# Performance work log

Measured on AMD Instinct MI355X. Metric: run time of the kernel, lower is better.

The kernel has to match this reference:

```python
import jax, jax.numpy as jnp
import numpy as np
import math

B, C, HH, WW = 4, 256, 64, 64
NUM_HEADS = 4
GROUPS = 8
EPS = 1e-5


def setup_inputs() -> dict:
    key = jax.random.key(0)
    k1, k2, k3 = jax.random.split(key, 3)
    x = jax.random.normal(k1, (B, C, HH, WW), dtype=jnp.float32)
    gn_w = jnp.ones((C,), dtype=jnp.float32)
    gn_b = jnp.zeros((C,), dtype=jnp.float32)
    qkv_w = jax.random.normal(k2, (3 * C, C), dtype=jnp.float32) * (1.0 / math.sqrt(C))
    qkv_b = jnp.zeros((3 * C,), dtype=jnp.float32)
    proj_w = jax.random.normal(k3, (C, C), dtype=jnp.float32) * (1.0 / math.sqrt(C))
    proj_b = jnp.zeros((C,), dtype=jnp.float32)
    return {"x": x, "gn_w": gn_w, "gn_b": gn_b, "qkv_w": qkv_w,
            "qkv_b": qkv_b, "proj_w": proj_w, "proj_b": proj_b}


def reference(x, gn_w, gn_b, qkv_w, qkv_b, proj_w, proj_b):
    b, c, h, w = x.shape
    nh = NUM_HEADS
    d = c // nh          # head dim = 64
    s = h * w            # sequence length = 4096

    # GroupNorm(8, c): normalize over (c//G, h, w) per group, biased variance
    xg = x.reshape(b, GROUPS, c // GROUPS, h, w)
    mu = xg.mean(axis=(2, 3, 4), keepdims=True)
    var = xg.var(axis=(2, 3, 4), keepdims=True)
    xn = ((xg - mu) * jax.lax.rsqrt(var + EPS)).reshape(b, c, h, w)
    xn = xn * gn_w[None, :, None, None] + gn_b[None, :, None, None]

    # 1x1 conv QKV == channel-wise matmul
    qkv = jnp.einsum('oc,bchw->bohw', qkv_w, xn) + qkv_b[None, :, None, None]
    qkv = qkv.reshape(b, 3, nh, d, s)
    q = jnp.transpose(qkv[:, 0], (0, 1, 3, 2))  # [b, nh, s, d]
    k = jnp.transpose(qkv[:, 1], (0, 1, 3, 2))
    v = jnp.transpose(qkv[:, 2], (0, 1, 3, 2))

    scale = 1.0 / math.sqrt(d)
    attn = jnp.einsum('bhqd,bhkd->bhqk', q, k) * scale  # [b, nh, s, s]
    attn = jax.nn.softmax(attn, axis=-1)
    out = jnp.einsum('bhqk,bhkd->bhqd', attn, v)        # [b, nh, s, d]

    out = jnp.transpose(out, (0, 1, 3, 2)).reshape(b, c, h, w)
    out = jnp.einsum('oc,bchw->bohw', proj_w, out) + proj_b[None, :, None, None]
    return out + x
```

## Files before the change

kernel.cpp:

```cpp
#include <hip/hip_runtime.h>
#include <hip/hip_bf16.h>

#define B_ 4
#define C_ 256
#define S_ 4096
#define NH_ 4
#define HD_ 64
#define LOG2E 1.4426950408889634f
#define QSC 0.18033688011112042f

typedef __attribute__((ext_vector_type(8))) short short8;
typedef __attribute__((ext_vector_type(4))) short short4v;
typedef __attribute__((ext_vector_type(4))) float f32x4;
typedef __attribute__((ext_vector_type(16))) float f32x16;
typedef __attribute__((ext_vector_type(4))) unsigned uint4v;

static __device__ __forceinline__ short f2bf(float f) {
  unsigned u = __builtin_bit_cast(unsigned, f);
  u += 0x7fffu + ((u >> 16) & 1u);
  return (short)(u >> 16);
}
static __device__ __forceinline__ float bf2f(short h) {
  unsigned u = ((unsigned)(unsigned short)h) << 16;
  return __builtin_bit_cast(float, u);
}

#if __has_builtin(__builtin_amdgcn_exp2f)
#define EXP2(x) __builtin_amdgcn_exp2f(x)
#else
#define EXP2(x) exp2f(x)
#endif

static __device__ __forceinline__ unsigned pkbf(float a, float b) {
  unsigned r;
  asm("v_cvt_pk_bf16_f32 %0, %1, %2" : "=v"(r) : "v"(a), "v"(b));
  return r;
}
static __device__ __forceinline__ void pl32swap(unsigned& a, unsigned& b) {
  asm volatile("v_permlane32_swap_b32 %0, %1" : "+v"(a), "+v"(b));
}
static __device__ __forceinline__ void gl_lds16(const short* g, char* l) {
  __builtin_amdgcn_global_load_lds(
      (const __attribute__((address_space(1))) void*)g,
      (__attribute__((address_space(3))) void*)l, 16, 0, 0);
}

__global__ __launch_bounds__(256) void k_pre(const float* __restrict__ x,
                                             const float* __restrict__ wq,
                                             const float* __restrict__ wp,
                                             float* __restrict__ part,
                                             short* __restrict__ oq,
                                             short* __restrict__ op) {
  int t = threadIdx.x;
  const float* p = x + (size_t)blockIdx.x * 16384;
  float s = 0.f, ss = 0.f;
  const float4* p4 = reinterpret_cast<const float4*>(p);
  for (int i = t; i < 4096; i += 256) {
    float4 v = p4[i];
    s += v.x + v.y + v.z + v.w;
    ss += v.x * v.x + v.y * v.y + v.z * v.z + v.w * v.w;
  }
  for (int m = 1; m < 64; m <<= 1) {
    s += __shfl_xor(s, m, 64);
    ss += __shfl_xor(ss, m, 64);
  }
  __shared__ float rs[4], rss[4];
  int w = t >> 6;
  if ((t & 63) == 0) { rs[w] = s; rss[w] = ss; }
  {
    int i = (blockIdx.x * 256 + t) * 4;
    const int n1 = 768 * 256;
    float sc = 1.f;
    const float* src;
    short* dst;
    if (i < n1) {
      src = wq + i; dst = oq + i;
      if (i < 256 * 256) sc = QSC;
    } else {
      src = wp + (i - n1); dst = op + (i - n1);
    }
    float4 v = *reinterpret_cast<const float4*>(src);
    short4v o;
    o[0] = f2bf(v.x * sc); o[1] = f2bf(v.y * sc);
    o[2] = f2bf(v.z * sc); o[3] = f2bf(v.w * sc);
    *reinterpret_cast<short4v*>(dst) = o;
  }
  __syncthreads();
  if (t == 0) {
    part[2 * blockIdx.x] = rs[0] + rs[1] + rs[2] + rs[3];
    part[2 * blockIdx.x + 1] = rss[0] + rss[1] + rss[2] + rss[3];
  }
}

__global__ __launch_bounds__(256) void k_gn_apply(const float* __restrict__ x,
                                                  const float* __restrict__ gw,
                                                  const float* __restrict__ gb,
                                                  const float* __restrict__ part,
                                                  short* __restrict__ xnt) {
  int st = blockIdx.x;
  int ct = blockIdx.y;
  int b = blockIdx.z;
  int t = threadIdx.x;
  __shared__ short T[64 * 72];
  __shared__ float smu[2], sri[2];
  int c0 = ct * 64, s0 = st * 64;
  if (t < 2) {
    int g = (c0 >> 5) + t;
    int base = b * 64 + g * 8;
    float s = 0.f, ss = 0.f;
    for (int j = 0; j < 8; j++) {
      s += part[2 * (base + j)];
      ss += part[2 * (base + j) + 1];
    }
    float inv = 1.f / (32.f * S_);
    float mu = s * inv;
    float var = ss * inv - mu * mu;
    smu[t] = mu;
    sri[t] = rsqrtf(var + 1e-5f);
  }
  __syncthreads();
  int r4 = t >> 4;
  int f4 = t & 15;
  for (int p = 0; p < 4; p++) {
    int r = p * 16 + r4;
    int c = c0 + r;
    int gl = r >> 5;
    float mu = smu[gl];
    float ri = sri[gl];
    float A = gw[c] * ri;
    float Bb = gb[c] - mu * A;
    float4 v = *reinterpret_cast<const float4*>(x + ((size_t)(b * C_ + c)) * S_ + s0 + f4 * 4);
    int sb = f4 * 4;
    T[(sb + 0) * 72 + r] = f2bf(v.x * A + Bb);
    T[(sb + 1) * 72 + r] = f2bf(v.y * A + Bb);
    T[(sb + 2) * 72 + r] = f2bf(v.z * A + Bb);
    T[(sb + 3) * 72 + r] = f2bf(v.w * A + Bb);
  }
  __syncthreads();
  for (int it = 0; it < 2; it++) {
    int cch = t + it * 256;
    int sl = cch >> 3, c8 = cch & 7;
    short8 v = *reinterpret_cast<short8*>(&T[sl * 72 + c8 * 8]);
    *reinterpret_cast<short8*>(xnt + ((size_t)(b * S_ + s0 + sl)) * C_ + c0 + c8 * 8) = v;
  }
}

template <int MODE, int NSP>
__global__ __launch_bounds__(256) void k_gemm(const short* __restrict__ Wbf,
                                              const short* __restrict__ Xt,
                                              const float* __restrict__ bias,
                                              const float* __restrict__ xres,
                                              short* __restrict__ q_sd,
                                              short* __restrict__ k_sd,
                                              short* __restrict__ v_ds,
                                              long op_stride,
                                              const float* __restrict__ lbufg,
                                              float* __restrict__ outp) {
  int tn = blockIdx.x;
  int tm = blockIdx.y;
  int b = blockIdx.z;
  int t = threadIdx.x;
  __shared__ short lds[4 * 64 * 72];
  short* Al = lds;
  short* Bl = lds + 128 * 40;
  int w = t >> 6, lane = t & 63;
  int wr = w >> 1, wc = w & 1;
  int l15 = lane & 15, l4 = lane >> 4;

  f32x4 acc[4][4];
  for (int m = 0; m < 4; m++)
    for (int n = 0; n < 4; n++)
      for (int j = 0; j < 4; j++) acc[m][n][j] = 0.f;

  const short* Arow = Wbf + (size_t)(tm * 128) * 256;
  const short* Brow = Xt + ((size_t)b * S_ + tn * 128) * 256;

  for (int kk = 0; kk < 256; kk += 32) {
    __syncthreads();
    for (int i = 0; i < 2; i++) {
      int cch = t + i * 256;
      int r = cch >> 2, c4 = cch & 3;
      short8 va = *reinterpret_cast<const short8*>(Arow + (size_t)r * 256 + kk + c4 * 8);
      *reinterpret_cast<short8*>(&Al[r * 40 + c4 * 8]) = va;
      short8 vbv;
      if (MODE == 0) {
        vbv = *reinterpret_cast<const short8*>(Brow + (size_t)r * 256 + kk + c4 * 8);
      } else {
        int c = kk + c4 * 8;
        int bh2 = b * 4 + (c >> 6);
        int d = c & 63;
        int s_glob = tn * 128 + r;
        size_t ro = ((size_t)bh2 * S_ + s_glob) * HD_ + d;
        float a8[8] = {0.f, 0.f, 0.f, 0.f, 0.f, 0.f, 0.f, 0.f};
        float l = 0.f;
#pragma unroll
        for (int i2 = 0; i2 < NSP; i2++) {
          short8 pv = *reinterpret_cast<const short8*>(Xt + (size_t)i2 * op_stride + ro);
#pragma unroll
          for (int j = 0; j < 8; j++) a8[j] += bf2f(pv[j]);
          l += lbufg[(size_t)(i2 * 16 + bh2) * S_ + s_glob];
        }
        float inv = 1.f / l;
#pragma unroll
        for (int j = 0; j < 8; j++) vbv[j] = f2bf(a8[j] * inv);
      }
      *reinterpret_cast<short8*>(&Bl[r * 40 + c4 * 8]) = vbv;
    }
    __syncthreads();
    short8 af[4], bf[4];
    for (int mt = 0; mt < 4; mt++)
      af[mt] = *reinterpret_cast<short8*>(&Al[(wr * 64 + mt * 16 + l15) * 40 + l4 * 8]);
    for (int nt = 0; nt < 4; nt++)
      bf[nt] = *reinterpret_cast<short8*>(&Bl[(wc * 64 + nt * 16 + l15) * 40 + l4 * 8]);
    for (int mt = 0; mt < 4; mt++)
      for (int nt = 0; nt < 4; nt++)
        acc[mt][nt] = __builtin_amdgcn_mfma_f32_16x16x32_bf16(af[mt], bf[nt], acc[mt][nt], 0, 0, 0);
  }
  __syncthreads();

  if (MODE == 0) {
    int o_base = tm * 128 + wr * 64;
    int tt = o_base >> 8;
    int h = (o_base >> 6) & 3;
    int s_base = tn * 128 + wc * 64;
    int bh = b * NH_ + h;
    if (tt == 2) {
      for (int mt = 0; mt < 4; mt++)
        for (int nt = 0; nt < 4; nt++)
          for (int i = 0; i < 4; i++) {
            int o = o_base + mt * 16 + l4 * 4 + i;
            int dd = o & 63;
            int s = s_base + nt * 16 + l15;
            float val = acc[mt][nt][i] + bias[o];
            v_ds[((size_t)bh * HD_ + dd) * S_ + s] = f2bf(val);
          }
    } else {
      float bsc = (tt == 0) ? QSC : 1.f;
      short* T = lds + w * (64 * 72);
      for (int mt = 0; mt < 4; mt++)
        for (int nt = 0; nt < 4; nt++)
          for (int i = 0; i < 4; i++) {
            int o = o_base + mt * 16 + l4 * 4 + i;
            int dd = mt * 16 + l4 * 4 + i;
            int sl = nt * 16 + l15;
            float val = acc[mt][nt][i] + bias[o] * bsc;
            T[sl * 72 + dd] = f2bf(val);
          }
      short* dst = (tt == 0) ? q_sd : k_sd;
      for (int it = 0; it < 8; it++) {
        int cch = lane + it * 64;
        int sl = cch >> 3, c8 = cch & 7;
        short8 v = *reinterpret_cast<short8*>(&T[sl * 72 + c8 * 8]);
        *reinterpret_cast<short8*>(dst + ((size_t)bh * S_ + s_base + sl) * HD_ + c8 * 8) = v;
      }
    }
  } else {
    for (int mt = 0; mt < 4; mt++) {
      int o = tm * 128 + wr * 64 + mt * 16 + l4 * 4;
      for (int nt = 0; nt < 4; nt++) {
        int s = tn * 128 + wc * 64 + nt * 16 + l15;
        for (int i = 0; i < 4; i++) {
          size_t off = ((size_t)(b * C_ + o + i)) * S_ + s;
          outp[off] = acc[mt][nt][i] + bias[o + i] + xres[off];
        }
      }
    }
  }
}

__global__ __launch_bounds__(256, 2) void k_attn(const short* __restrict__ q_sd,
                                                 const short* __restrict__ k_sd,
                                                 const short* __restrict__ v_ds,
                                                 short* __restrict__ op_base,
                                                 long op_stride,
                                                 float* __restrict__ lbuf,
                                                 int ntile, int lg) {
  int bid = blockIdx.x;
  int sk = bid & ((1 << lg) - 1);
  int bh = (bid >> lg) & 15;
  int qt = bid >> (lg + 4);
  int t = threadIdx.x, w = t >> 6, lane = t & 63;
  int l31 = lane & 31, hi = lane >> 5, hi8 = hi * 8;
  int qb = qt * 256 + w * 64;

  __shared__ char smem[32768];

  int wb = __builtin_amdgcn_readfirstlane(w) << 10;

  int r8 = t >> 3, s8 = t & 7;
  int sw8 = (s8 ^ (r8 & 7)) * 8;
  const short* kb = k_sd + ((size_t)bh * S_ + (size_t)sk * ntile * 64) * HD_;
  const short* vbg = v_ds + (size_t)bh * HD_ * S_ + sk * ntile * 64;
  int koff0 = r8 * 64 + sw8;
  int koff1 = koff0 + 32 * 64;
  size_t voff0 = (size_t)r8 * S_ + sw8;
  size_t voff1 = voff0 + (size_t)32 * S_;

#define STAGE(bsel, ti)                                                        \
  do {                                                                         \
    const short* kt_ = kb + (size_t)(ti) * (64 * HD_);                         \
    const short* vt_ = vbg + (ti) * 64;                                        \
    char* lb_ = smem + ((bsel) << 14) + wb;                                    \
    gl_lds16(kt_ + koff0, lb_);                                                \
    gl_lds16(kt_ + koff1, lb_ + 4096);                                         \
    gl_lds16(vt_ + voff0, lb_ + 8192);                                         \
    gl_lds16(vt_ + voff1, lb_ + 12288);                                        \
  } while (0)

  const short* qpA = q_sd + ((size_t)bh * S_ + qb + l31) * HD_ + hi8;
  short8 qfA[4], qfB[4];
#pragma unroll
  for (int sl = 0; sl < 4; sl++) {
    qfA[sl] = *reinterpret_cast<const short8*>(qpA + sl * 16);
    qfB[sl] = *reinterpret_cast<const short8*>(qpA + 32 * HD_ + sl * 16);
  }

  int x7 = l31 & 7;
  int rb0 = l31 * 128;

  f32x16 OA0, OA1, OB0, OB1;
#pragma unroll
  for (int r = 0; r < 16; r++) { OA0[r] = 0.f; OA1[r] = 0.f; OB0[r] = 0.f; OB1[r] = 0.f; }
  float lA = 0.f, lB = 0.f;

  STAGE(0, 0);
  if (ntile > 1) STAGE(1, 1);
  asm volatile("s_waitcnt vmcnt(0)" ::: "memory");
  __builtin_amdgcn_s_barrier();
  asm volatile("" ::: "memory");

#define MKPA(pa, s0, s1)                                                       \
  do {                                                                         \
    unsigned c0 = pkbf(s0[0], s0[1]), c1 = pkbf(s0[2], s0[3]);                 \
    unsigned c2 = pkbf(s0[4], s0[5]), c3 = pkbf(s0[6], s0[7]);                 \
    pl32swap(c0, c2); pl32swap(c1, c3);                                        \
    uint4v u0; u0[0] = c0; u0[1] = c1; u0[2] = c2; u0[3] = c3;                 \
    pa[0] = __builtin_bit_cast(short8, u0);                                    \
    unsigned c4 = pkbf(s0[8], s0[9]), c5 = pkbf(s0[10], s0[11]);               \
    unsigned c6 = pkbf(s0[12], s0[13]), c7 = pkbf(s0[14], s0[15]);             \
    pl32swap(c4, c6); pl32swap(c5, c7);                                        \
    uint4v u1; u1[0] = c4; u1[1] = c5; u1[2] = c6; u1[3] = c7;                 \
    pa[1] = __builtin_bit_cast(short8, u1);                                    \
    unsigned d0 = pkbf(s1[0], s1[1]), d1 = pkbf(s1[2], s1[3]);                 \
    unsigned d2 = pkbf(s1[4], s1[5]), d3 = pkbf(s1[6], s1[7]);                 \
    pl32swap(d0, d2); pl32swap(d1, d3);                                        \
    uint4v u2; u2[0] = d0; u2[1] = d1; u2[2] = d2; u2[3] = d3;                 \
    pa[2] = __builtin_bit_cast(short8, u2);                                    \
    unsigned d4 = pkbf(s1[8], s1[9]), d5 = pkbf(s1[10], s1[11]);               \
    unsigned d6 = pkbf(s1[12], s1[13]), d7 = pkbf(s1[14], s1[15]);             \
    pl32swap(d4, d6); pl32swap(d5, d7);                                        \
    uint4v u3; u3[0] = d4; u3[1] = d5; u3[2] = d6; u3[3] = d7;                 \
    pa[3] = __builtin_bit_cast(short8, u3);                                    \
  } while (0)

  for (int it = 0; it < ntile; it++) {
    char* cur = smem + ((it & 1) << 14);

    f32x16 sA0, sA1, sB0, sB1;
#pragma unroll
    for (int r = 0; r < 16; r++) { sA0[r] = 0.f; sA1[r] = 0.f; sB0[r] = 0.f; sB1[r] = 0.f; }
    __builtin_amdgcn_s_setprio(1);
#pragma unroll
    for (int sl = 0; sl < 4; sl++) {
      int so = ((sl * 2 + hi) ^ x7) << 4;
      short8 kf0 = *reinterpret_cast<short8*>(cur + rb0 + so);
      short8 kf1 = *reinterpret_cast<short8*>(cur + 4096 + rb0 + so);
      sA0 = __builtin_amdgcn_mfma_f32_32x32x16_bf16(kf0, qfA[sl], sA0, 0, 0, 0);
      sB0 = __builtin_amdgcn_mfma_f32_32x32x16_bf16(kf0, qfB[sl], sB0, 0, 0, 0);
      sA1 = __builtin_amdgcn_mfma_f32_32x32x16_bf16(kf1, qfA[sl], sA1, 0, 0, 0);
      sB1 = __builtin_amdgcn_mfma_f32_32x32x16_bf16(kf1, qfB[sl], sB1, 0, 0, 0);
    }
    __builtin_amdgcn_s_setprio(0);

#pragma unroll
    for (int r = 0; r < 16; r++) sA0[r] = EXP2(sA0[r]);
#pragma unroll
    for (int r = 0; r < 16; r++) sA1[r] = EXP2(sA1[r]);
#pragma unroll
    for (int r = 0; r < 16; r++) sB0[r] = EXP2(sB0[r]);
#pragma unroll
    for (int r = 0; r < 16; r++) sB1[r] = EXP2(sB1[r]);
    {
      float a0 = 0.f, a1 = 0.f, a2 = 0.f, a3 = 0.f;
      float b0 = 0.f, b1 = 0.f, b2 = 0.f, b3 = 0.f;
#pragma unroll
      for (int r = 0; r < 16; r += 4) {
        a0 += sA0[r]; a1 += sA0[r + 1]; a2 += sA0[r + 2]; a3 += sA0[r + 3];
        a0 += sA1[r]; a1 += sA1[r + 1]; a2 += sA1[r + 2]; a3 += sA1[r + 3];
        b0 += sB0[r]; b1 += sB0[r + 1]; b2 += sB0[r + 2]; b3 += sB0[r + 3];
        b0 += sB1[r]; b1 += sB1[r + 1]; b2 += sB1[r + 2]; b3 += sB1[r + 3];
      }
      float rsA = (a0 + a1) + (a2 + a3);
      float rsB = (b0 + b1) + (b2 + b3);
      rsA += __shfl_xor(rsA, 32, 64);
      rsB += __shfl_xor(rsB, 32, 64);
      lA += rsA;
      lB += rsB;
    }

    short8 paA[4], paB[4];
    MKPA(paA, sA0, sA1);
    MKPA(paB, sB0, sB1);

    __builtin_amdgcn_s_setprio(1);
#pragma unroll
    for (int ks = 0; ks < 4; ks++) {
      int so = ((ks * 2 + hi) ^ x7) << 4;
      short8 vf0 = *reinterpret_cast<short8*>(cur + 8192 + rb0 + so);
      short8 vf1 = *reinterpret_cast<short8*>(cur + 12288 + rb0 + so);
      OA0 = __builtin_amdgcn_mfma_f32_32x32x16_bf16(vf0, paA[ks], OA0, 0, 0, 0);
      OB0 = __builtin_amdgcn_mfma_f32_32x32x16_bf16(vf0, paB[ks], OB0, 0, 0, 0);
      OA1 = __builtin_amdgcn_mfma_f32_32x32x16_bf16(vf1, paA[ks], OA1, 0, 0, 0);
      OB1 = __builtin_amdgcn_mfma_f32_32x32x16_bf16(vf1, paB[ks], OB1, 0, 0, 0);
    }
    __builtin_amdgcn_s_setprio(0);

    if (it + 1 < ntile) {
      __builtin_amdgcn_s_barrier();
      if (it + 2 < ntile) {
        STAGE(it & 1, it + 2);
        asm volatile("s_waitcnt vmcnt(4)" ::: "memory");
      } else {
        asm volatile("s_waitcnt vmcnt(0)" ::: "memory");
      }
      __builtin_amdgcn_s_barrier();
      asm volatile("" ::: "memory");
    }
  }

  short* optrA = op_base + (size_t)sk * op_stride + ((size_t)bh * S_ + qb + l31) * HD_;
  short* optrB = optrA + 32 * HD_;
#pragma unroll
  for (int qd = 0; qd < 4; qd++) {
    short4v a0, a1, b0v, b1v;
#pragma unroll
    for (int i = 0; i < 4; i++) {
      a0[i] = f2bf(OA0[qd * 4 + i]);
      a1[i] = f2bf(OA1[qd * 4 + i]);
      b0v[i] = f2bf(OB0[qd * 4 + i]);
      b1v[i] = f2bf(OB1[qd * 4 + i]);
    }
    int d0 = qd * 8 + hi * 4;
    *reinterpret_cast<short4v*>(optrA + d0) = a0;
    *reinterpret_cast<short4v*>(optrA + 32 + d0) = a1;
    *reinterpret_cast<short4v*>(optrB + d0) = b0v;
    *reinterpret_cast<short4v*>(optrB + 32 + d0) = b1v;
  }
  if (hi == 0) {
    lbuf[(size_t)(sk * 16 + bh) * S_ + qb + l31] = lA;
    lbuf[(size_t)(sk * 16 + bh) * S_ + qb + 32 + l31] = lB;
  }
#undef STAGE
#undef MKPA
}

extern "C" void kernel_launch(void* const* d_in, const int* in_sizes, int n_in,
                              void* d_out, int out_size, void* d_ws, size_t ws_size,
                              hipStream_t stream) {
  const float* x      = (const float*)d_in[0];
  const float* gn_w   = (const float*)d_in[1];
  const float* gn_b   = (const float*)d_in[2];
  const float* qkv_w  = (const float*)d_in[3];
  const float* qkv_b  = (const float*)d_in[4];
  const float* proj_w = (const float*)d_in[5];
  const float* proj_b = (const float*)d_in[6];
  char* ws = (char*)d_ws;
  float* part  = (float*)(ws + 2048);
  short* wqkv  = (short*)(ws + 4096);
  short* wproj = (short*)(ws + 397312);
  short* xnt   = (short*)(ws + 528384);
  short* q_sd  = (short*)(ws + 8916992);
  short* k_sd  = (short*)(ws + 17305600);
  short* v_ds  = (short*)(ws + 25694208);
  float* outp  = (float*)d_out;

  const size_t need4 = 42471424ULL + 4ULL * 8388608ULL + 4ULL * 16 * 4096 * 4;
  int lg;
  short* op_base;
  long op_stride;
  float* lbuf;
  if (ws_size >= need4) {
    lg = 2;
    op_base = (short*)(ws + 42471424);
    op_stride = 8388608 / 2;
    lbuf = (float*)(ws + 42471424 + 4ULL * 8388608ULL);
  } else {
    lg = 1;
    op_base = xnt;
    op_stride = (42471424 - 528384) / 2;
    lbuf = (float*)(ws + 50860032);
  }
  int NS = 1 << lg;

  k_pre<<<256, 256, 0, stream>>>(x, qkv_w, proj_w, part, wqkv, wproj);
  k_gn_apply<<<dim3(64, 4, 4), 256, 0, stream>>>(x, gn_w, gn_b, part, xnt);
  k_gemm<0, 0><<<dim3(32, 6, 4), 256, 0, stream>>>(wqkv, xnt, qkv_b, nullptr, q_sd, k_sd, v_ds,
                                                   0, nullptr, nullptr);
  k_attn<<<16 * 16 * NS, 256, 0, stream>>>(q_sd, k_sd, v_ds, op_base, op_stride, lbuf,
                                           64 >> lg, lg);
  if (NS == 4)
    k_gemm<1, 4><<<dim3(32, 2, 4), 256, 0, stream>>>(wproj, op_base, proj_b, x, nullptr, nullptr,
                                                     nullptr, op_stride, lbuf, outp);
  else
    k_gemm<1, 2><<<dim3(32, 2, 4), 256, 0, stream>>>(wproj, op_base, proj_b, x, nullptr, nullptr,
                                                     nullptr, op_stride, lbuf, outp);
}
```

Baseline: 135.1 us.

## Halve attention query tile per wave and double grid for higher occupancy

Each wave now processes 32 query rows instead of 64, cutting accumulator and score registers in half, and launch bounds are raised to four blocks per CU. The grid doubles to cover the same queries. The aim is more resident waves to hide latency, at the cost of loading each K/V tile twice as often, halving the reuse of staged K/V per block.

```diff
diff --git a/kernel.cpp b/kernel.cpp
--- a/kernel.cpp
+++ b/kernel.cpp
@@ -268,7 +268,7 @@
   }
 }
 
-__global__ __launch_bounds__(256, 2) void k_attn(const short* __restrict__ q_sd,
+__global__ __launch_bounds__(256, 4) void k_attn(const short* __restrict__ q_sd,
                                                  const short* __restrict__ k_sd,
                                                  const short* __restrict__ v_ds,
                                                  short* __restrict__ op_base,
@@ -281,7 +281,7 @@
   int qt = bid >> (lg + 4);
   int t = threadIdx.x, w = t >> 6, lane = t & 63;
   int l31 = lane & 31, hi = lane >> 5, hi8 = hi * 8;
-  int qb = qt * 256 + w * 64;
+  int qb = qt * 128 + w * 32;
 
   __shared__ char smem[32768];
 
@@ -307,21 +307,18 @@
     gl_lds16(vt_ + voff1, lb_ + 12288);                                        \
   } while (0)
 
-  const short* qpA = q_sd + ((size_t)bh * S_ + qb + l31) * HD_ + hi8;
-  short8 qfA[4], qfB[4];
-#pragma unroll
-  for (int sl = 0; sl < 4; sl++) {
-    qfA[sl] = *reinterpret_cast<const short8*>(qpA + sl * 16);
-    qfB[sl] = *reinterpret_cast<const short8*>(qpA + 32 * HD_ + sl * 16);
-  }
+  const short* qp = q_sd + ((size_t)bh * S_ + qb + l31) * HD_ + hi8;
+  short8 qf[4];
+#pragma unroll
+  for (int sl = 0; sl < 4; sl++) qf[sl] = *reinterpret_cast<const short8*>(qp + sl * 16);
 
   int x7 = l31 & 7;
   int rb0 = l31 * 128;
 
-  f32x16 OA0, OA1, OB0, OB1;
-#pragma unroll
-  for (int r = 0; r < 16; r++) { OA0[r] = 0.f; OA1[r] = 0.f; OB0[r] = 0.f; OB1[r] = 0.f; }
-  float lA = 0.f, lB = 0.f;
+  f32x16 Oacc0, Oacc1;
+#pragma unroll
+  for (int r = 0; r < 16; r++) { Oacc0[r] = 0.f; Oacc1[r] = 0.f; }
+  float l_run = 0.f;
 
   STAGE(0, 0);
   if (ntile > 1) STAGE(1, 1);
@@ -329,78 +326,62 @@
   __builtin_amdgcn_s_barrier();
   asm volatile("" ::: "memory");
 
-#define MKPA(pa, s0, s1)                                                       \
-  do {                                                                         \
-    unsigned c0 = pkbf(s0[0], s0[1]), c1 = pkbf(s0[2], s0[3]);                 \
-    unsigned c2 = pkbf(s0[4], s0[5]), c3 = pkbf(s0[6], s0[7]);                 \
-    pl32swap(c0, c2); pl32swap(c1, c3);                                        \
-    uint4v u0; u0[0] = c0; u0[1] = c1; u0[2] = c2; u0[3] = c3;                 \
-    pa[0] = __builtin_bit_cast(short8, u0);                                    \
-    unsigned c4 = pkbf(s0[8], s0[9]), c5 = pkbf(s0[10], s0[11]);               \
-    unsigned c6 = pkbf(s0[12], s0[13]), c7 = pkbf(s0[14], s0[15]);             \
-    pl32swap(c4, c6); pl32swap(c5, c7);                                        \
-    uint4v u1; u1[0] = c4; u1[1] = c5; u1[2] = c6; u1[3] = c7;                 \
-    pa[1] = __builtin_bit_cast(short8, u1);                                    \
-    unsigned d0 = pkbf(s1[0], s1[1]), d1 = pkbf(s1[2], s1[3]);                 \
-    unsigned d2 = pkbf(s1[4], s1[5]), d3 = pkbf(s1[6], s1[7]);                 \
-    pl32swap(d0, d2); pl32swap(d1, d3);                                        \
-    uint4v u2; u2[0] = d0; u2[1] = d1; u2[2] = d2; u2[3] = d3;                 \
-    pa[2] = __builtin_bit_cast(short8, u2);                                    \
-    unsigned d4 = pkbf(s1[8], s1[9]), d5 = pkbf(s1[10], s1[11]);               \
-    unsigned d6 = pkbf(s1[12], s1[13]), d7 = pkbf(s1[14], s1[15]);             \
-    pl32swap(d4, d6); pl32swap(d5, d7);                                        \
-    uint4v u3; u3[0] = d4; u3[1] = d5; u3[2] = d6; u3[3] = d7;                 \
-    pa[3] = __builtin_bit_cast(short8, u3);                                    \
-  } while (0)
-
   for (int it = 0; it < ntile; it++) {
     char* cur = smem + ((it & 1) << 14);
 
-    f32x16 sA0, sA1, sB0, sB1;
-#pragma unroll
-    for (int r = 0; r < 16; r++) { sA0[r] = 0.f; sA1[r] = 0.f; sB0[r] = 0.f; sB1[r] = 0.f; }
+    f32x16 st0, st1;
+#pragma unroll
+    for (int r = 0; r < 16; r++) { st0[r] = 0.f; st1[r] = 0.f; }
     __builtin_amdgcn_s_setprio(1);
 #pragma unroll
     for (int sl = 0; sl < 4; sl++) {
       int so = ((sl * 2 + hi) ^ x7) << 4;
       short8 kf0 = *reinterpret_cast<short8*>(cur + rb0 + so);
       short8 kf1 = *reinterpret_cast<short8*>(cur + 4096 + rb0 + so);
-      sA0 = __builtin_amdgcn_mfma_f32_32x32x16_bf16(kf0, qfA[sl], sA0, 0, 0, 0);
-      sB0 = __builtin_amdgcn_mfma_f32_32x32x16_bf16(kf0, qfB[sl], sB0, 0, 0, 0);
-      sA1 = __builtin_amdgcn_mfma_f32_32x32x16_bf16(kf1, qfA[sl], sA1, 0, 0, 0);
-      sB1 = __builtin_amdgcn_mfma_f32_32x32x16_bf16(kf1, qfB[sl], sB1, 0, 0, 0);
+      st0 = __builtin_amdgcn_mfma_f32_32x32x16_bf16(kf0, qf[sl], st0, 0, 0, 0);
+      st1 = __builtin_amdgcn_mfma_f32_32x32x16_bf16(kf1, qf[sl], st1, 0, 0, 0);
     }
     __builtin_amdgcn_s_setprio(0);
 
 #pragma unroll
-    for (int r = 0; r < 16; r++) sA0[r] = EXP2(sA0[r]);
-#pragma unroll
-    for (int r = 0; r < 16; r++) sA1[r] = EXP2(sA1[r]);
-#pragma unroll
-    for (int r = 0; r < 16; r++) sB0[r] = EXP2(sB0[r]);
-#pragma unroll
-    for (int r = 0; r < 16; r++) sB1[r] = EXP2(sB1[r]);
+    for (int r = 0; r < 16; r++) st0[r] = EXP2(st0[r]);
+#pragma unroll
+    for (int r = 0; r < 16; r++) st1[r] = EXP2(st1[r]);
     {
       float a0 = 0.f, a1 = 0.f, a2 = 0.f, a3 = 0.f;
-      float b0 = 0.f, b1 = 0.f, b2 = 0.f, b3 = 0.f;
 #pragma unroll
       for (int r = 0; r < 16; r += 4) {
-        a0 += sA0[r]; a1 += sA0[r + 1]; a2 += sA0[r + 2]; a3 += sA0[r + 3];
-        a0 += sA1[r]; a1 += sA1[r + 1]; a2 += sA1[r + 2]; a3 += sA1[r + 3];
-        b0 += sB0[r]; b1 += sB0[r + 1]; b2 += sB0[r + 2]; b3 += sB0[r + 3];
-        b0 += sB1[r]; b1 += sB1[r + 1]; b2 += sB1[r + 2]; b3 += sB1[r + 3];
+        a0 += st0[r]; a1 += st0[r + 1]; a2 += st0[r + 2]; a3 += st0[r + 3];
+        a0 += st1[r]; a1 += st1[r + 1]; a2 += st1[r + 2]; a3 += st1[r + 3];
       }
-      float rsA = (a0 + a1) + (a2 + a3);
-      float rsB = (b0 + b1) + (b2 + b3);
-      rsA += __shfl_xor(rsA, 32, 64);
-      rsB += __shfl_xor(rsB, 32, 64);
-      lA += rsA;
-      lB += rsB;
-    }
-
-    short8 paA[4], paB[4];
-    MKPA(paA, sA0, sA1);
-    MKPA(paB, sB0, sB1);
+      float rs = (a0 + a1) + (a2 + a3);
+      rs += __shfl_xor(rs, 32, 64);
+      l_run += rs;
+    }
+
+    short8 pa[4];
+    {
+      unsigned c0 = pkbf(st0[0], st0[1]), c1 = pkbf(st0[2], st0[3]);
+      unsigned c2 = pkbf(st0[4], st0[5]), c3 = pkbf(st0[6], st0[7]);
+      pl32swap(c0, c2); pl32swap(c1, c3);
+      uint4v u0; u0[0] = c0; u0[1] = c1; u0[2] = c2; u0[3] = c3;
+      pa[0] = __builtin_bit_cast(short8, u0);
+      unsigned c4 = pkbf(st0[8], st0[9]), c5 = pkbf(st0[10], st0[11]);
+      unsigned c6 = pkbf(st0[12], st0[13]), c7 = pkbf(st0[14], st0[15]);
+      pl32swap(c4, c6); pl32swap(c5, c7);
+      uint4v u1; u1[0] = c4; u1[1] = c5; u1[2] = c6; u1[3] = c7;
+      pa[1] = __builtin_bit_cast(short8, u1);
+      unsigned d0 = pkbf(st1[0], st1[1]), d1 = pkbf(st1[2], st1[3]);
+      unsigned d2 = pkbf(st1[4], st1[5]), d3 = pkbf(st1[6], st1[7]);
+      pl32swap(d0, d2); pl32swap(d1, d3);
+      uint4v u2; u2[0] = d0; u2[1] = d1; u2[2] = d2; u2[3] = d3;
+      pa[2] = __builtin_bit_cast(short8, u2);
+      unsigned d4 = pkbf(st1[8], st1[9]), d5 = pkbf(st1[10], st1[11]);
+      unsigned d6 = pkbf(st1[12], st1[13]), d7 = pkbf(st1[14], st1[15]);
+      pl32swap(d4, d6); pl32swap(d5, d7);
+      uint4v u3; u3[0] = d4; u3[1] = d5; u3[2] = d6; u3[3] = d7;
+      pa[3] = __builtin_bit_cast(short8, u3);
+    }
 
     __builtin_amdgcn_s_setprio(1);
 #pragma unroll
@@ -408,10 +389,8 @@
       int so = ((ks * 2 + hi) ^ x7) << 4;
       short8 vf0 = *reinterpret_cast<short8*>(cur + 8192 + rb0 + so);
       short8 vf1 = *reinterpret_cast<short8*>(cur + 12288 + rb0 + so);
-      OA0 = __builtin_amdgcn_mfma_f32_32x32x16_bf16(vf0, paA[ks], OA0, 0, 0, 0);
-      OB0 = __builtin_amdgcn_mfma_f32_32x32x16_bf16(vf0, paB[ks], OB0, 0, 0, 0);
-      OA1 = __builtin_amdgcn_mfma_f32_32x32x16_bf16(vf1, paA[ks], OA1, 0, 0, 0);
-      OB1 = __builtin_amdgcn_mfma_f32_32x32x16_bf16(vf1, paB[ks], OB1, 0, 0, 0);
+      Oacc0 = __builtin_amdgcn_mfma_f32_32x32x16_bf16(vf0, pa[ks], Oacc0, 0, 0, 0);
+      Oacc1 = __builtin_amdgcn_mfma_f32_32x32x16_bf16(vf1, pa[ks], Oacc1, 0, 0, 0);
     }
     __builtin_amdgcn_s_setprio(0);
 
@@ -428,30 +407,21 @@
     }
   }
 
-  short* optrA = op_base + (size_t)sk * op_stride + ((size_t)bh * S_ + qb + l31) * HD_;
-  short* optrB = optrA + 32 * HD_;
+  short* optr = op_base + (size_t)sk * op_stride + ((size_t)bh * S_ + qb + l31) * HD_;
 #pragma unroll
   for (int qd = 0; qd < 4; qd++) {
-    short4v a0, a1, b0v, b1v;
+    short4v o0, o1;
 #pragma unroll
     for (int i = 0; i < 4; i++) {
-      a0[i] = f2bf(OA0[qd * 4 + i]);
-      a1[i] = f2bf(OA1[qd * 4 + i]);
-      b0v[i] = f2bf(OB0[qd * 4 + i]);
-      b1v[i] = f2bf(OB1[qd * 4 + i]);
+      o0[i] = f2bf(Oacc0[qd * 4 + i]);
+      o1[i] = f2bf(Oacc1[qd * 4 + i]);
     }
     int d0 = qd * 8 + hi * 4;
-    *reinterpret_cast<short4v*>(optrA + d0) = a0;
-    *reinterpret_cast<short4v*>(optrA + 32 + d0) = a1;
-    *reinterpret_cast<short4v*>(optrB + d0) = b0v;
-    *reinterpret_cast<short4v*>(optrB + 32 + d0) = b1v;
-  }
-  if (hi == 0) {
-    lbuf[(size_t)(sk * 16 + bh) * S_ + qb + l31] = lA;
-    lbuf[(size_t)(sk * 16 + bh) * S_ + qb + 32 + l31] = lB;
-  }
+    *reinterpret_cast<short4v*>(optr + d0) = o0;
+    *reinterpret_cast<short4v*>(optr + 32 + d0) = o1;
+  }
+  if (hi == 0) lbuf[(size_t)(sk * 16 + bh) * S_ + qb + l31] = l_run;
 #undef STAGE
-#undef MKPA
 }
 
 extern "C" void kernel_launch(void* const* d_in, const int* in_sizes, int n_in,
@@ -496,7 +466,7 @@
   k_gn_apply<<<dim3(64, 4, 4), 256, 0, stream>>>(x, gn_w, gn_b, part, xnt);
   k_gemm<0, 0><<<dim3(32, 6, 4), 256, 0, stream>>>(wqkv, xnt, qkv_b, nullptr, q_sd, k_sd, v_ds,
                                                    0, nullptr, nullptr);
-  k_attn<<<16 * 16 * NS, 256, 0, stream>>>(q_sd, k_sd, v_ds, op_base, op_stride, lbuf,
+  k_attn<<<32 * 16 * NS, 256, 0, stream>>>(q_sd, k_sd, v_ds, op_base, op_stride, lbuf,
                                            64 >> lg, lg);
   if (NS == 4)
     k_gemm<1, 4><<<dim3(32, 2, 4), 256, 0, stream>>>(wproj, op_base, proj_b, x, nullptr, nullptr,
```

Measured after the change: 139.5 us. 1.03x slower.

## Split attention KV tile into two halves to cut registers and raise occupancy

Applied to the files above, without the earlier changes.

Each 64-key tile is now processed as two 32-key halves, each running QK^T, exp2, row-sum, bf16 packing and PV MFMA, so only two score accumulators are live instead of four. Launch bounds go from 2 to 3 waves per SIMD to use the lower register pressure, the cross-half row-sum shuffle is moved out of the loop to once at the end, and V offsets become 32-bit ints. The risk is spills under the tighter register budget and less MFMA/exp overlap within a wave.

```diff
diff --git a/kernel.cpp b/kernel.cpp
--- a/kernel.cpp
+++ b/kernel.cpp
@@ -268,7 +268,7 @@
   }
 }
 
-__global__ __launch_bounds__(256, 2) void k_attn(const short* __restrict__ q_sd,
+__global__ __launch_bounds__(256, 3) void k_attn(const short* __restrict__ q_sd,
                                                  const short* __restrict__ k_sd,
                                                  const short* __restrict__ v_ds,
                                                  short* __restrict__ op_base,
@@ -293,8 +293,8 @@
   const short* vbg = v_ds + (size_t)bh * HD_ * S_ + sk * ntile * 64;
   int koff0 = r8 * 64 + sw8;
   int koff1 = koff0 + 32 * 64;
-  size_t voff0 = (size_t)r8 * S_ + sw8;
-  size_t voff1 = voff0 + (size_t)32 * S_;
+  int voff0 = r8 * S_ + sw8;
+  int voff1 = voff0 + 32 * S_;
 
 #define STAGE(bsel, ti)                                                        \
   do {                                                                         \
@@ -329,91 +329,80 @@
   __builtin_amdgcn_s_barrier();
   asm volatile("" ::: "memory");
 
-#define MKPA(pa, s0, s1)                                                       \
-  do {                                                                         \
-    unsigned c0 = pkbf(s0[0], s0[1]), c1 = pkbf(s0[2], s0[3]);                 \
-    unsigned c2 = pkbf(s0[4], s0[5]), c3 = pkbf(s0[6], s0[7]);                 \
-    pl32swap(c0, c2); pl32swap(c1, c3);                                        \
-    uint4v u0; u0[0] = c0; u0[1] = c1; u0[2] = c2; u0[3] = c3;                 \
-    pa[0] = __builtin_bit_cast(short8, u0);                                    \
-    unsigned c4 = pkbf(s0[8], s0[9]), c5 = pkbf(s0[10], s0[11]);               \
-    unsigned c6 = pkbf(s0[12], s0[13]), c7 = pkbf(s0[14], s0[15]);             \
-    pl32swap(c4, c6); pl32swap(c5, c7);                                        \
-    uint4v u1; u1[0] = c4; u1[1] = c5; u1[2] = c6; u1[3] = c7;                 \
-    pa[1] = __builtin_bit_cast(short8, u1);                                    \
-    unsigned d0 = pkbf(s1[0], s1[1]), d1 = pkbf(s1[2], s1[3]);                 \
-    unsigned d2 = pkbf(s1[4], s1[5]), d3 = pkbf(s1[6], s1[7]);                 \
-    pl32swap(d0, d2); pl32swap(d1, d3);                                        \
-    uint4v u2; u2[0] = d0; u2[1] = d1; u2[2] = d2; u2[3] = d3;                 \
-    pa[2] = __builtin_bit_cast(short8, u2);                                    \
-    unsigned d4 = pkbf(s1[8], s1[9]), d5 = pkbf(s1[10], s1[11]);               \
-    unsigned d6 = pkbf(s1[12], s1[13]), d7 = pkbf(s1[14], s1[15]);             \
-    pl32swap(d4, d6); pl32swap(d5, d7);                                        \
-    uint4v u3; u3[0] = d4; u3[1] = d5; u3[2] = d6; u3[3] = d7;                 \
-    pa[3] = __builtin_bit_cast(short8, u3);                                    \
-  } while (0)
-
   for (int it = 0; it < ntile; it++) {
     char* cur = smem + ((it & 1) << 14);
 
-    f32x16 sA0, sA1, sB0, sB1;
-#pragma unroll
-    for (int r = 0; r < 16; r++) { sA0[r] = 0.f; sA1[r] = 0.f; sB0[r] = 0.f; sB1[r] = 0.f; }
-    __builtin_amdgcn_s_setprio(1);
-#pragma unroll
-    for (int sl = 0; sl < 4; sl++) {
-      int so = ((sl * 2 + hi) ^ x7) << 4;
-      short8 kf0 = *reinterpret_cast<short8*>(cur + rb0 + so);
-      short8 kf1 = *reinterpret_cast<short8*>(cur + 4096 + rb0 + so);
-      sA0 = __builtin_amdgcn_mfma_f32_32x32x16_bf16(kf0, qfA[sl], sA0, 0, 0, 0);
-      sB0 = __builtin_amdgcn_mfma_f32_32x32x16_bf16(kf0, qfB[sl], sB0, 0, 0, 0);
-      sA1 = __builtin_amdgcn_mfma_f32_32x32x16_bf16(kf1, qfA[sl], sA1, 0, 0, 0);
-      sB1 = __builtin_amdgcn_mfma_f32_32x32x16_bf16(kf1, qfB[sl], sB1, 0, 0, 0);
-    }
-    __builtin_amdgcn_s_setprio(0);
-
-#pragma unroll
-    for (int r = 0; r < 16; r++) sA0[r] = EXP2(sA0[r]);
-#pragma unroll
-    for (int r = 0; r < 16; r++) sA1[r] = EXP2(sA1[r]);
-#pragma unroll
-    for (int r = 0; r < 16; r++) sB0[r] = EXP2(sB0[r]);
-#pragma unroll
-    for (int r = 0; r < 16; r++) sB1[r] = EXP2(sB1[r]);
-    {
-      float a0 = 0.f, a1 = 0.f, a2 = 0.f, a3 = 0.f;
-      float b0 = 0.f, b1 = 0.f, b2 = 0.f, b3 = 0.f;
-#pragma unroll
-      for (int r = 0; r < 16; r += 4) {
-        a0 += sA0[r]; a1 += sA0[r + 1]; a2 += sA0[r + 2]; a3 += sA0[r + 3];
-        a0 += sA1[r]; a1 += sA1[r + 1]; a2 += sA1[r + 2]; a3 += sA1[r + 3];
-        b0 += sB0[r]; b1 += sB0[r + 1]; b2 += sB0[r + 2]; b3 += sB0[r + 3];
-        b0 += sB1[r]; b1 += sB1[r + 1]; b2 += sB1[r + 2]; b3 += sB1[r + 3];
-      }
-      float rsA = (a0 + a1) + (a2 + a3);
-      float rsB = (b0 + b1) + (b2 + b3);
-      rsA += __shfl_xor(rsA, 32, 64);
-      rsB += __shfl_xor(rsB, 32, 64);
-      lA += rsA;
-      lB += rsB;
-    }
-
-    short8 paA[4], paB[4];
-    MKPA(paA, sA0, sA1);
-    MKPA(paB, sB0, sB1);
-
-    __builtin_amdgcn_s_setprio(1);
-#pragma unroll
-    for (int ks = 0; ks < 4; ks++) {
-      int so = ((ks * 2 + hi) ^ x7) << 4;
-      short8 vf0 = *reinterpret_cast<short8*>(cur + 8192 + rb0 + so);
-      short8 vf1 = *reinterpret_cast<short8*>(cur + 12288 + rb0 + so);
-      OA0 = __builtin_amdgcn_mfma_f32_32x32x16_bf16(vf0, paA[ks], OA0, 0, 0, 0);
-      OB0 = __builtin_amdgcn_mfma_f32_32x32x16_bf16(vf0, paB[ks], OB0, 0, 0, 0);
-      OA1 = __builtin_amdgcn_mfma_f32_32x32x16_bf16(vf1, paA[ks], OA1, 0, 0, 0);
-      OB1 = __builtin_amdgcn_mfma_f32_32x32x16_bf16(vf1, paB[ks], OB1, 0, 0, 0);
-    }
-    __builtin_amdgcn_s_setprio(0);
+#pragma unroll
+    for (int h = 0; h < 2; h++) {
+      f32x16 SA, SB;
+#pragma unroll
+      for (int r = 0; r < 16; r++) { SA[r] = 0.f; SB[r] = 0.f; }
+      __builtin_amdgcn_s_setprio(1);
+#pragma unroll
+      for (int sl = 0; sl < 4; sl++) {
+        int so = ((sl * 2 + hi) ^ x7) << 4;
+        short8 kf = *reinterpret_cast<short8*>(cur + h * 4096 + rb0 + so);
+        SA = __builtin_amdgcn_mfma_f32_32x32x16_bf16(kf, qfA[sl], SA, 0, 0, 0);
+        SB = __builtin_amdgcn_mfma_f32_32x32x16_bf16(kf, qfB[sl], SB, 0, 0, 0);
+      }
+      __builtin_amdgcn_s_setprio(0);
+
+#pragma unroll
+      for (int r = 0; r < 16; r++) SA[r] = EXP2(SA[r]);
+#pragma unroll
+      for (int r = 0; r < 16; r++) SB[r] = EXP2(SB[r]);
+      {
+        float a0 = 0.f, a1 = 0.f, a2 = 0.f, a3 = 0.f;
+        float b0 = 0.f, b1 = 0.f, b2 = 0.f, b3 = 0.f;
+#pragma unroll
+        for (int r = 0; r < 16; r += 4) {
+          a0 += SA[r]; a1 += SA[r + 1]; a2 += SA[r + 2]; a3 += SA[r + 3];
+          b0 += SB[r]; b1 += SB[r + 1]; b2 += SB[r + 2]; b3 += SB[r + 3];
+        }
+        lA += (a0 + a1) + (a2 + a3);
+        lB += (b0 + b1) + (b2 + b3);
+      }
+
+      short8 paA0, paA1, paB0, paB1;
+      {
+        unsigned c0 = pkbf(SA[0], SA[1]), c1 = pkbf(SA[2], SA[3]);
+        unsigned c2 = pkbf(SA[4], SA[5]), c3 = pkbf(SA[6], SA[7]);
+        pl32swap(c0, c2); pl32swap(c1, c3);
+        uint4v u0; u0[0] = c0; u0[1] = c1; u0[2] = c2; u0[3] = c3;
+        paA0 = __builtin_bit_cast(short8, u0);
+        unsigned c4 = pkbf(SA[8], SA[9]), c5 = pkbf(SA[10], SA[11]);
+        unsigned c6 = pkbf(SA[12], SA[13]), c7 = pkbf(SA[14], SA[15]);
+        pl32swap(c4, c6); pl32swap(c5, c7);
+        uint4v u1; u1[0] = c4; u1[1] = c5; u1[2] = c6; u1[3] = c7;
+        paA1 = __builtin_bit_cast(short8, u1);
+        unsigned d0 = pkbf(SB[0], SB[1]), d1 = pkbf(SB[2], SB[3]);
+        unsigned d2 = pkbf(SB[4], SB[5]), d3 = pkbf(SB[6], SB[7]);
+        pl32swap(d0, d2); pl32swap(d1, d3);
+        uint4v u2; u2[0] = d0; u2[1] = d1; u2[2] = d2; u2[3] = d3;
+        paB0 = __builtin_bit_cast(short8, u2);
+        unsigned d4 = pkbf(SB[8], SB[9]), d5 = pkbf(SB[10], SB[11]);
+        unsigned d6 = pkbf(SB[12], SB[13]), d7 = pkbf(SB[14], SB[15]);
+        pl32swap(d4, d6); pl32swap(d5, d7);
+        uint4v u3; u3[0] = d4; u3[1] = d5; u3[2] = d6; u3[3] = d7;
+        paB1 = __builtin_bit_cast(short8, u3);
+      }
+
+      __builtin_amdgcn_s_setprio(1);
+#pragma unroll
+      for (int k2 = 0; k2 < 2; k2++) {
+        int ks = h * 2 + k2;
+        int so = ((ks * 2 + hi) ^ x7) << 4;
+        short8 vf0 = *reinterpret_cast<short8*>(cur + 8192 + rb0 + so);
+        short8 vf1 = *reinterpret_cast<short8*>(cur + 12288 + rb0 + so);
+        short8 pA = k2 ? paA1 : paA0;
+        short8 pB = k2 ? paB1 : paB0;
+        OA0 = __builtin_amdgcn_mfma_f32_32x32x16_bf16(vf0, pA, OA0, 0, 0, 0);
+        OB0 = __builtin_amdgcn_mfma_f32_32x32x16_bf16(vf0, pB, OB0, 0, 0, 0);
+        OA1 = __builtin_amdgcn_mfma_f32_32x32x16_bf16(vf1, pA, OA1, 0, 0, 0);
+        OB1 = __builtin_amdgcn_mfma_f32_32x32x16_bf16(vf1, pB, OB1, 0, 0, 0);
+      }
+      __builtin_amdgcn_s_setprio(0);
+    }
 
     if (it + 1 < ntile) {
       __builtin_amdgcn_s_barrier();
@@ -428,6 +417,8 @@
     }
   }
 
+  lA += __shfl_xor(lA, 32, 64);
+  lB += __shfl_xor(lB, 32, 64);
   short* optrA = op_base + (size_t)sk * op_stride + ((size_t)bh * S_ + qb + l31) * HD_;
   short* optrB = optrA + 32 * HD_;
 #pragma unroll
@@ -451,7 +442,6 @@
     lbuf[(size_t)(sk * 16 + bh) * S_ + qb + 32 + l31] = lB;
   }
 #undef STAGE
-#undef MKPA
 }
 
 extern "C" void kernel_launch(void* const* d_in, const int* in_sizes, int n_in,
```

New measurement: 323.3 us. 139% more time.

## Use direct global-to-LDS loads with XOR swizzle in GEMM; fix attention split to two

Applied to the files above, without the earlier changes.

The GEMM tile loads for the weight operand and, in the QKV GEMM, the activation operand now go straight from global memory into LDS through gl_lds16 with an XOR-swizzled layout. This replaces register-staged copies with padded rows and is meant to cut VGPR traffic and LDS bank conflicts. The attention kernel no longer chooses a 4-way key split based on workspace size and always uses a 2-way split with 512 blocks. This removes the 4-way partial reduction work in the projection GEMM, but it also lowers parallelism in the attention kernel whenever the larger workspace was available.

```diff
diff --git a/kernel.cpp b/kernel.cpp
--- a/kernel.cpp
+++ b/kernel.cpp
@@ -161,11 +161,13 @@
   int b = blockIdx.z;
   int t = threadIdx.x;
   __shared__ short lds[4 * 64 * 72];
-  short* Al = lds;
-  short* Bl = lds + 128 * 40;
+  char* Al = (char*)lds;
+  char* Bl = (char*)lds + 8192;
+  short* Blp = lds + 4096;
   int w = t >> 6, lane = t & 63;
   int wr = w >> 1, wc = w & 1;
   int l15 = lane & 15, l4 = lane >> 4;
+  int wbg = __builtin_amdgcn_readfirstlane(w) << 10;
 
   f32x4 acc[4][4];
   for (int m = 0; m < 4; m++)
@@ -175,17 +177,22 @@
   const short* Arow = Wbf + (size_t)(tm * 128) * 256;
   const short* Brow = Xt + ((size_t)b * S_ + tn * 128) * 256;
 
+  int r0 = t >> 2, c40 = t & 3;
+  int sw0 = (c40 ^ ((r0 >> 1) & 3)) * 8;
+  int r1 = (t + 256) >> 2;
+  int sw1 = (c40 ^ ((r1 >> 1) & 3)) * 8;
+
   for (int kk = 0; kk < 256; kk += 32) {
     __syncthreads();
-    for (int i = 0; i < 2; i++) {
-      int cch = t + i * 256;
-      int r = cch >> 2, c4 = cch & 3;
-      short8 va = *reinterpret_cast<const short8*>(Arow + (size_t)r * 256 + kk + c4 * 8);
-      *reinterpret_cast<short8*>(&Al[r * 40 + c4 * 8]) = va;
-      short8 vbv;
-      if (MODE == 0) {
-        vbv = *reinterpret_cast<const short8*>(Brow + (size_t)r * 256 + kk + c4 * 8);
-      } else {
+    gl_lds16(Arow + (size_t)r0 * 256 + kk + sw0, Al + wbg);
+    gl_lds16(Arow + (size_t)r1 * 256 + kk + sw1, Al + 4096 + wbg);
+    if (MODE == 0) {
+      gl_lds16(Brow + (size_t)r0 * 256 + kk + sw0, Bl + wbg);
+      gl_lds16(Brow + (size_t)r1 * 256 + kk + sw1, Bl + 4096 + wbg);
+    } else {
+      for (int i = 0; i < 2; i++) {
+        int cch = t + i * 256;
+        int r = cch >> 2, c4 = cch & 3;
         int c = kk + c4 * 8;
         int bh2 = b * 4 + (c >> 6);
         int d = c & 63;
@@ -201,17 +208,27 @@
           l += lbufg[(size_t)(i2 * 16 + bh2) * S_ + s_glob];
         }
         float inv = 1.f / l;
+        short8 vbv;
 #pragma unroll
         for (int j = 0; j < 8; j++) vbv[j] = f2bf(a8[j] * inv);
+        *reinterpret_cast<short8*>(&Blp[r * 40 + c4 * 8]) = vbv;
       }
-      *reinterpret_cast<short8*>(&Bl[r * 40 + c4 * 8]) = vbv;
-    }
+    }
+    asm volatile("s_waitcnt vmcnt(0)" ::: "memory");
     __syncthreads();
+
     short8 af[4], bf[4];
-    for (int mt = 0; mt < 4; mt++)
-      af[mt] = *reinterpret_cast<short8*>(&Al[(wr * 64 + mt * 16 + l15) * 40 + l4 * 8]);
-    for (int nt = 0; nt < 4; nt++)
-      bf[nt] = *reinterpret_cast<short8*>(&Bl[(wc * 64 + nt * 16 + l15) * 40 + l4 * 8]);
+    for (int mt = 0; mt < 4; mt++) {
+      int row = wr * 64 + mt * 16 + l15;
+      af[mt] = *reinterpret_cast<short8*>(Al + row * 64 + ((l4 ^ ((row >> 1) & 3)) << 4));
+    }
+    for (int nt = 0; nt < 4; nt++) {
+      int row = wc * 64 + nt * 16 + l15;
+      if (MODE == 0)
+        bf[nt] = *reinterpret_cast<short8*>(Bl + row * 64 + ((l4 ^ ((row >> 1) & 3)) << 4));
+      else
+        bf[nt] = *reinterpret_cast<short8*>(&Blp[row * 40 + l4 * 8]);
+    }
     for (int mt = 0; mt < 4; mt++)
       for (int nt = 0; nt < 4; nt++)
         acc[mt][nt] = __builtin_amdgcn_mfma_f32_16x16x32_bf16(af[mt], bf[nt], acc[mt][nt], 0, 0, 0);
@@ -274,11 +291,11 @@
                                                  short* __restrict__ op_base,
                                                  long op_stride,
                                                  float* __restrict__ lbuf,
-                                                 int ntile, int lg) {
+                                                 int ntile) {
   int bid = blockIdx.x;
-  int sk = bid & ((1 << lg) - 1);
-  int bh = (bid >> lg) & 15;
-  int qt = bid >> (lg + 4);
+  int qt = bid >> 5;
+  int bh = (bid >> 1) & 15;
+  int sk = bid & 1;
   int t = threadIdx.x, w = t >> 6, lane = t & 63;
   int l31 = lane & 31, hi = lane >> 5, hi8 = hi * 8;
   int qb = qt * 256 + w * 64;
@@ -472,36 +489,16 @@
   short* q_sd  = (short*)(ws + 8916992);
   short* k_sd  = (short*)(ws + 17305600);
   short* v_ds  = (short*)(ws + 25694208);
+  short* op_base = xnt;
+  long op_stride = (42471424 - 528384) / 2;
+  float* lbuf  = (float*)(ws + 50860032);
   float* outp  = (float*)d_out;
-
-  const size_t need4 = 42471424ULL + 4ULL * 8388608ULL + 4ULL * 16 * 4096 * 4;
-  int lg;
-  short* op_base;
-  long op_stride;
-  float* lbuf;
-  if (ws_size >= need4) {
-    lg = 2;
-    op_base = (short*)(ws + 42471424);
-    op_stride = 8388608 / 2;
-    lbuf = (float*)(ws + 42471424 + 4ULL * 8388608ULL);
-  } else {
-    lg = 1;
-    op_base = xnt;
-    op_stride = (42471424 - 528384) / 2;
-    lbuf = (float*)(ws + 50860032);
-  }
-  int NS = 1 << lg;
 
   k_pre<<<256, 256, 0, stream>>>(x, qkv_w, proj_w, part, wqkv, wproj);
   k_gn_apply<<<dim3(64, 4, 4), 256, 0, stream>>>(x, gn_w, gn_b, part, xnt);
   k_gemm<0, 0><<<dim3(32, 6, 4), 256, 0, stream>>>(wqkv, xnt, qkv_b, nullptr, q_sd, k_sd, v_ds,
                                                    0, nullptr, nullptr);
-  k_attn<<<16 * 16 * NS, 256, 0, stream>>>(q_sd, k_sd, v_ds, op_base, op_stride, lbuf,
-                                           64 >> lg, lg);
-  if (NS == 4)
-    k_gemm<1, 4><<<dim3(32, 2, 4), 256, 0, stream>>>(wproj, op_base, proj_b, x, nullptr, nullptr,
-                                                     nullptr, op_stride, lbuf, outp);
-  else
-    k_gemm<1, 2><<<dim3(32, 2, 4), 256, 0, stream>>>(wproj, op_base, proj_b, x, nullptr, nullptr,
-                                                     nullptr, op_stride, lbuf, outp);
-}
+  k_attn<<<512, 256, 0, stream>>>(q_sd, k_sd, v_ds, op_base, op_stride, lbuf, 32);
+  k_gemm<1, 2><<<dim3(32, 2, 4), 256, 0, stream>>>(wproj, op_base, proj_b, x, nullptr, nullptr,
+                                                   nullptr, op_stride, lbuf, outp);
+}
```

Result: faster. 125.8 us (median of 5 runs) (-6.8%).
